# Optimization experiments

Hardware: AMD Instinct MI355X
Metric: run time of the kernel (lower is better)

The kernel has to match this reference:

```python
import jax, jax.numpy as jnp
import numpy as np

SR = 44100
ATTACK_MS = 10.0
RELEASE_MS = 100.0
RATIO_DN = 66.7
RATIO_UP = 0.1
KNEE = 0.1
UP_RANGE_DB = 36.0
TMIN = -40.0
TMAX = 0.0
A_AT = float(np.exp(-1.0 / (ATTACK_MS * SR / 1000.0)))
A_REL = float(np.exp(-1.0 / (RELEASE_MS * SR / 1000.0)))


def smooth_log_level(rect_db):
    # rect_db: [B, N]. Leaky integrator with input-dependent attack/release coeff.
    def step(curr, v):  # curr, v: [B]
        alpha = jnp.where(v > curr, A_AT, A_REL)
        new = alpha * curr + (1.0 - alpha) * v
        return new, new
    _, lv = jax.lax.scan(step, rect_db[:, 0], rect_db.T)  # lv: [N, B]
    return lv.T


def setup_inputs() -> dict:
    key = jax.random.key(0)
    k1, k2 = jax.random.split(key)
    x = jax.random.normal(k1, (16, 441000), dtype=jnp.float32)
    threshold = jax.random.uniform(k2, (16, 1), dtype=jnp.float32)
    depth = jnp.ones((16, 1), dtype=jnp.float32)
    return {"x": x, "threshold": threshold, "depth": depth}


def reference(x, threshold, depth):
    # mode == 'peak'
    rect = jnp.abs(x)
    rect_db = 20.0 * jnp.log10(rect + 1e-8)
    level_db = smooth_log_level(rect_db)  # [B, N]
    thresh_db = TMIN + threshold * (TMAX - TMIN)  # [B, 1]
    diff_dn = level_db - thresh_db
    gain_dn_db = jnp.where(
        diff_dn > -KNEE,
        -(1.0 - 1.0 / RATIO_DN) * 0.5 * (diff_dn + KNEE + jnp.sqrt((diff_dn - KNEE) ** 2 + 1e-4)),
        jnp.zeros_like(diff_dn),
    )
    diff_up = thresh_db - level_db
    raw_gain_up_db = jnp.where(
        diff_up > -KNEE,
        (1.0 - RATIO_UP) * 0.5 * (diff_up + KNEE + jnp.sqrt((diff_up - KNEE) ** 2 + 1e-4)),
        jnp.zeros_like(diff_up),
    )
    gain_up_db = jnp.minimum(raw_gain_up_db, UP_RANGE_DB)
    gain_db = (gain_dn_db + gain_up_db) * depth
    gain = 10.0 ** (gain_db / 20.0)
    return x * gain
```

## Files before the change

kernel.cpp:

```cpp
#include <hip/hip_runtime.h>
#include <math.h>

#define N_SAMP 441000
#define BATCH  16
#define N_OCT  55125
#define OPAD   55296
#define NMG    13824
#define MGF    576
#define MGB    2304
#define NWAVE  54

#define A_AT  0.9977349953069123f
#define A_REL 0.9997732683378945f
#define OMA_AT  (1.0f - A_AT)
#define OMA_REL (1.0f - A_REL)

typedef float vf4 __attribute__((ext_vector_type(4)));

static __device__ __forceinline__ float rect_db_f(float xv) {
    return 6.020599913279624f * log2f(fabsf(xv) + 1e-8f);
}
static __device__ __forceinline__ float step_v(float s, float v) {
    return fmaxf(fmaf(A_AT, s, OMA_AT * v), fmaf(A_REL, s, OMA_REL * v));
}
static __device__ __forceinline__ float max3f(float a, float b, float c) {
    float d;
    asm("v_max3_f32 %0, %1, %2, %3" : "=v"(d) : "v"(a), "v"(b), "v"(c));
    return d;
}
static __device__ __forceinline__ float gain_mul(float s, float th, float dp) {
    float ddn = s - th;
    float gdn = 0.0f;
    if (ddn > -0.1f) {
        float dm = ddn - 0.1f;
        gdn = -0.4925037481259370f * (ddn + 0.1f + sqrtf(fmaf(dm, dm, 1e-4f)));
    }
    float dup = th - s;
    float gup = 0.0f;
    if (dup > -0.1f) {
        float um = dup - 0.1f;
        gup = 0.45f * (dup + 0.1f + sqrtf(fmaf(um, um, 1e-4f)));
    }
    gup = fminf(gup, 36.0f);
    return exp2f((gdn + gup) * dp * 0.1660964047443681f);
}

__global__ __launch_bounds__(256) void coef8_kernel(const float* __restrict__ x,
                                                    float* __restrict__ K) {
    int l = blockIdx.x * 256 + threadIdx.x;
    int slot = l & 3, b = (l >> 2) & 15, mg = l >> 6;
    int o = mg * 4 + slot;
    if (o >= N_OCT) return;
    const float4* xp = (const float4*)(x + (size_t)b * N_SAMP + (size_t)o * 8);
    float4 xa = xp[0], xb = xp[1];
    float vv[8];
    vv[0] = rect_db_f(xa.x); vv[1] = rect_db_f(xa.y);
    vv[2] = rect_db_f(xa.z); vv[3] = rect_db_f(xa.w);
    vv[4] = rect_db_f(xb.x); vv[5] = rect_db_f(xb.y);
    vv[6] = rect_db_f(xb.z); vv[7] = rect_db_f(xb.w);
    float c[9];
    c[0] = OMA_REL * vv[0];
    c[1] = OMA_AT * vv[0];
    #pragma unroll
    for (int j = 1; j < 8; ++j) {
        float p = OMA_AT * vv[j], q = OMA_REL * vv[j];
        c[j + 1] = fmaf(A_AT, c[j], p);
        #pragma unroll
        for (int m = j; m >= 1; --m)
            c[m] = fmaxf(fmaf(A_AT, c[m - 1], p), fmaf(A_REL, c[m], q));
        c[0] = fmaf(A_REL, c[0], q);
    }
    float* kp = K + (size_t)mg * MGF + (b * 4 + slot);
    #pragma unroll
    for (int pl = 0; pl < 9; ++pl) kp[pl * 64] = c[pl];
}

__global__ __launch_bounds__(64, 1) void scan8_kernel(const float* __restrict__ Kf,
                                                      const float* __restrict__ x,
                                                      float* __restrict__ lvl) {
    int wb = blockIdx.x;
    int xcd = wb & 7, jj = wb >> 3;
    int w = (xcd < 6 ? xcd * 7 : 42 + (xcd - 6) * 6) + jj;
    const int lane = threadIdx.x;
    const int grp = lane >> 4, b = lane & 15;
    const int k = 4 * w + grp;

    constexpr double dAT = 0.9977349953069123, dRL = 0.9997732683378945;
    constexpr double dAT2 = dAT * dAT, dAT4 = dAT2 * dAT2;
    constexpr double dRL2 = dRL * dRL, dRL4 = dRL2 * dRL2;
    const float S0 = (float)(dRL4 * dRL4);
    const float S1 = (float)(dAT * dRL4 * dRL2 * dRL);
    const float S2 = (float)(dAT2 * dRL4 * dRL2);
    const float S3 = (float)(dAT2 * dAT * dRL4 * dRL);
    const float S4 = (float)(dAT4 * dRL4);
    const float S5 = (float)(dAT4 * dAT * dRL2 * dRL);
    const float S6 = (float)(dAT4 * dAT2 * dRL2);
    const float S7 = (float)(dAT4 * dAT2 * dAT * dRL);
    const float S8 = (float)(dAT4 * dAT4);

    vf4 R0[9], R1[9], R2[9], R3[9];
    vf4 lv;
    float s;
    unsigned voff;
    float* lq;
    float* dq = lvl + (size_t)16 * OPAD + lane * 4;

#define LDB(R) do {                                                                              \
    asm volatile("global_load_dwordx4 %0, %1, %2 offset:0"    : "=v"(R[0]) : "v"(voff), "s"(Kf)); \
    asm volatile("global_load_dwordx4 %0, %1, %2 offset:256"  : "=v"(R[1]) : "v"(voff), "s"(Kf)); \
    asm volatile("global_load_dwordx4 %0, %1, %2 offset:512"  : "=v"(R[2]) : "v"(voff), "s"(Kf)); \
    asm volatile("global_load_dwordx4 %0, %1, %2 offset:768"  : "=v"(R[3]) : "v"(voff), "s"(Kf)); \
    asm volatile("global_load_dwordx4 %0, %1, %2 offset:1024" : "=v"(R[4]) : "v"(voff), "s"(Kf)); \
    asm volatile("global_load_dwordx4 %0, %1, %2 offset:1280" : "=v"(R[5]) : "v"(voff), "s"(Kf)); \
    asm volatile("global_load_dwordx4 %0, %1, %2 offset:1536" : "=v"(R[6]) : "v"(voff), "s"(Kf)); \
    asm volatile("global_load_dwordx4 %0, %1, %2 offset:1792" : "=v"(R[7]) : "v"(voff), "s"(Kf)); \
    asm volatile("global_load_dwordx4 %0, %1, %2 offset:2048" : "=v"(R[8]) : "v"(voff), "s"(Kf)); \
    voff += MGB;                                                                                  \
} while (0)

#define WAITP() do {                                       \
    asm volatile("s_waitcnt vmcnt(27)" ::: "memory");      \
    __builtin_amdgcn_sched_barrier(0);                     \
} while (0)

#define CMP(R) do {                                        \
    _Pragma("unroll")                                      \
    for (int _e = 0; _e < 4; ++_e) {                       \
        float c0 = fmaf(S0, s, R[0][_e]);                  \
        float c1 = fmaf(S1, s, R[1][_e]);                  \
        float c2 = fmaf(S2, s, R[2][_e]);                  \
        float c3 = fmaf(S3, s, R[3][_e]);                  \
        float c4 = fmaf(S4, s, R[4][_e]);                  \
        float c5 = fmaf(S5, s, R[5][_e]);                  \
        float c6 = fmaf(S6, s, R[6][_e]);                  \
        float c7 = fmaf(S7, s, R[7][_e]);                  \
        float c8 = fmaf(S8, s, R[8][_e]);                  \
        s = max3f(max3f(c0, c1, c2), max3f(c3, c4, c5), max3f(c6, c7, c8)); \
        lv[_e] = s;                                        \
    }                                                      \
} while (0)

#define PH_W(R) do { WAITP(); CMP(R); LDB(R); } while (0)
#define PH_E(R) do { WAITP(); CMP(R);                      \
    lq[0] = lv[0]; lq[16] = lv[1]; lq[32] = lv[2]; lq[48] = lv[3]; lq += 64; \
    LDB(R); } while (0)
#define PH_D(R) do { WAITP(); CMP(R); {                    \
    float* _sp = ((unsigned)(sb - kw) < 64u) ? lq : dq;    \
    _sp[0] = lv[0]; _sp[16] = lv[1]; _sp[32] = lv[2]; _sp[48] = lv[3]; }   \
    lq += 64; ++sb; LDB(R); } while (0)

    if (w >= 4) {
        const int g0 = (k - 16) * 64;
        s = rect_db_f(x[(size_t)b * N_SAMP + (size_t)g0 * 32]);
        asm volatile("" :: "v"(s));
        voff = (unsigned)g0 * MGB + (unsigned)b * 16u;
        LDB(R0); LDB(R1); LDB(R2); LDB(R3);
        #pragma clang loop unroll(disable)
        for (int it = 0; it < 256; ++it) { PH_W(R0); PH_W(R1); PH_W(R2); PH_W(R3); }
        lq = lvl + (size_t)k * 256 * 16 + b;
        #pragma clang loop unroll(disable)
        for (int it = 0; it < 16; ++it) { PH_E(R0); PH_E(R1); PH_E(R2); PH_E(R3); }
    } else {
        const int nit = (4 * w + 4) * 16;
        s = rect_db_f(x[(size_t)b * N_SAMP]);
        asm volatile("" :: "v"(s));
        voff = (unsigned)b * 16u;
        int sb = 0;
        const unsigned kw = (unsigned)(k << 6);
        lq = lvl + b;
        LDB(R0); LDB(R1); LDB(R2); LDB(R3);
        #pragma clang loop unroll(disable)
        for (int it = 0; it < nit; ++it) { PH_D(R0); PH_D(R1); PH_D(R2); PH_D(R3); }
    }
    asm volatile("s_waitcnt vmcnt(0)" ::: "memory");

#undef LDB
#undef WAITP
#undef CMP
#undef PH_W
#undef PH_E
#undef PH_D
}

__global__ __launch_bounds__(256) void out8_kernel(const float* __restrict__ x,
                                                   const float* __restrict__ lvl,
                                                   const float* __restrict__ thr,
                                                   const float* __restrict__ dep,
                                                   float* __restrict__ out) {
    int o = blockIdx.x * 256 + threadIdx.x;
    int b = blockIdx.y;
    if (o >= N_OCT) return;
    const float4* xp = (const float4*)(x + (size_t)b * N_SAMP + (size_t)o * 8);
    float4 xa = xp[0], xb = xp[1];
    float v0 = rect_db_f(xa.x), v1 = rect_db_f(xa.y);
    float v2 = rect_db_f(xa.z), v3 = rect_db_f(xa.w);
    float v4 = rect_db_f(xb.x), v5 = rect_db_f(xb.y);
    float v6 = rect_db_f(xb.z), v7 = rect_db_f(xb.w);
    float s = (o == 0) ? v0 : lvl[(size_t)(o - 1) * 16 + b];
    float l0 = step_v(s, v0);
    float l1 = step_v(l0, v1);
    float l2 = step_v(l1, v2);
    float l3 = step_v(l2, v3);
    float l4 = step_v(l3, v4);
    float l5 = step_v(l4, v5);
    float l6 = step_v(l5, v6);
    float l7 = step_v(l6, v7);
    float th = fmaf(thr[b], 40.0f, -40.0f);
    float dp = dep[b];
    float4 oa, ob;
    oa.x = xa.x * gain_mul(l0, th, dp);
    oa.y = xa.y * gain_mul(l1, th, dp);
    oa.z = xa.z * gain_mul(l2, th, dp);
    oa.w = xa.w * gain_mul(l3, th, dp);
    ob.x = xb.x * gain_mul(l4, th, dp);
    ob.y = xb.y * gain_mul(l5, th, dp);
    ob.z = xb.z * gain_mul(l6, th, dp);
    ob.w = xb.w * gain_mul(l7, th, dp);
    float4* op = (float4*)(out + (size_t)b * N_SAMP + (size_t)o * 8);
    op[0] = oa;
    op[1] = ob;
}

__global__ __launch_bounds__(64) void scan_fused(const float* __restrict__ x,
                                                 const float* __restrict__ thr,
                                                 const float* __restrict__ dep,
                                                 float* __restrict__ out) {
    int t = blockIdx.x * 64 + threadIdx.x;
    const int NCH = 54, CH = 8192, WM = 32768;
    if (t >= BATCH * NCH) return;
    int b = t / NCH, k = t - b * NCH;
    int start = k * CH, end = min(start + CH, N_SAMP), w0 = max(start - WM, 0);
    const float* xr = x + (size_t)b * N_SAMP;
    float th = fmaf(thr[b], 40.0f, -40.0f);
    float dp = dep[b];
    float s = rect_db_f(xr[w0]);
    for (int j = w0; j < start; ++j) s = step_v(s, rect_db_f(xr[j]));
    float* orow = out + (size_t)b * N_SAMP;
    for (int j = start; j < end; ++j) {
        float xv = xr[j];
        s = step_v(s, rect_db_f(xv));
        orow[j] = xv * gain_mul(s, th, dp);
    }
}

extern "C" void kernel_launch(void* const* d_in, const int* in_sizes, int n_in,
                              void* d_out, int out_size, void* d_ws, size_t ws_size,
                              hipStream_t stream) {
    const float* x   = (const float*)d_in[0];
    const float* thr = (const float*)d_in[1];
    const float* dep = (const float*)d_in[2];
    float* out = (float*)d_out;

    const size_t k_bytes   = (size_t)NMG * MGF * sizeof(float);
    const size_t lvl_bytes = ((size_t)16 * OPAD + 512) * sizeof(float);

    if (ws_size >= k_bytes + lvl_bytes) {
        float* K   = (float*)d_ws;
        float* lvl = (float*)((char*)d_ws + k_bytes);
        coef8_kernel<<<(NMG * 64) / 256, 256, 0, stream>>>(x, K);
        scan8_kernel<<<NWAVE, 64, 0, stream>>>(K, x, lvl);
        dim3 gpar((N_OCT + 255) / 256, BATCH);
        out8_kernel<<<gpar, 256, 0, stream>>>(x, lvl, thr, dep, out);
    } else {
        scan_fused<<<(BATCH * 54 + 63) / 64, 64, 0, stream>>>(x, thr, dep, out);
    }
}
```

Before: 253.3 us.

## Stage scan coefficients through LDS with a 7-deep async global-to-LDS pipeline

Replaces the register-resident 4-stage global_load_dwordx4 ring in the sequential scan with global_load_lds staging into a 7-slot shared-memory ring. Each phase then reads the next block from LDS into a double-buffered register set. The goal is a deeper prefetch without the VGPR cost, so the latency-bound serial max-plus scan stalls less on memory. The level buffer layout also changes from [octet][batch] to [batch][octet], so the stores become contiguous vf4 writes, and out8_kernel indexing is updated to match. This adds LDS traffic, extra waitcnt bookkeeping and complex loop-count arithmetic that could mis-cover the tail.

Result: slower. 329.5 us (+30.1%).

```diff
diff --git a/kernel.cpp b/kernel.cpp
--- a/kernel.cpp
+++ b/kernel.cpp
@@ -78,6 +78,8 @@
 __global__ __launch_bounds__(64, 1) void scan8_kernel(const float* __restrict__ Kf,
                                                       const float* __restrict__ x,
                                                       float* __restrict__ lvl) {
+    __shared__ vf4 smem[7 * 576];
+
     int wb = blockIdx.x;
     int xcd = wb & 7, jj = wb >> 3;
     int w = (xcd < 6 ? xcd * 7 : 42 + (xcd - 6) * 6) + jj;
@@ -98,29 +100,25 @@
     const float S7 = (float)(dAT4 * dAT2 * dAT * dRL);
     const float S8 = (float)(dAT4 * dAT4);
 
-    vf4 R0[9], R1[9], R2[9], R3[9];
+    vf4 rA[9], rB[9];
     vf4 lv;
     float s;
-    unsigned voff;
-    float* lq;
+    const char* gp;
+    float* lq = lvl;
     float* dq = lvl + (size_t)16 * OPAD + lane * 4;
-
-#define LDB(R) do {                                                                              \
-    asm volatile("global_load_dwordx4 %0, %1, %2 offset:0"    : "=v"(R[0]) : "v"(voff), "s"(Kf)); \
-    asm volatile("global_load_dwordx4 %0, %1, %2 offset:256"  : "=v"(R[1]) : "v"(voff), "s"(Kf)); \
-    asm volatile("global_load_dwordx4 %0, %1, %2 offset:512"  : "=v"(R[2]) : "v"(voff), "s"(Kf)); \
-    asm volatile("global_load_dwordx4 %0, %1, %2 offset:768"  : "=v"(R[3]) : "v"(voff), "s"(Kf)); \
-    asm volatile("global_load_dwordx4 %0, %1, %2 offset:1024" : "=v"(R[4]) : "v"(voff), "s"(Kf)); \
-    asm volatile("global_load_dwordx4 %0, %1, %2 offset:1280" : "=v"(R[5]) : "v"(voff), "s"(Kf)); \
-    asm volatile("global_load_dwordx4 %0, %1, %2 offset:1536" : "=v"(R[6]) : "v"(voff), "s"(Kf)); \
-    asm volatile("global_load_dwordx4 %0, %1, %2 offset:1792" : "=v"(R[7]) : "v"(voff), "s"(Kf)); \
-    asm volatile("global_load_dwordx4 %0, %1, %2 offset:2048" : "=v"(R[8]) : "v"(voff), "s"(Kf)); \
-    voff += MGB;                                                                                  \
-} while (0)
-
-#define WAITP() do {                                       \
-    asm volatile("s_waitcnt vmcnt(27)" ::: "memory");      \
-    __builtin_amdgcn_sched_barrier(0);                     \
+    int sb = 0;
+    unsigned kw = 0;
+
+#define GLLDS(GPTR, LIDX)                                                        \
+    __builtin_amdgcn_global_load_lds(                                            \
+        (const __attribute__((address_space(1))) void*)(GPTR),                   \
+        (__attribute__((address_space(3))) void*)&smem[(LIDX)], 16, 0, 0)
+
+#define STAGE(SLOT) do {                                                         \
+    _Pragma("unroll")                                                            \
+    for (int _j = 0; _j < 9; ++_j)                                               \
+        GLLDS(gp + _j * 256, (SLOT) * 576 + _j * 64);                            \
+    gp += MGB;                                                                   \
 } while (0)
 
 #define CMP(R) do {                                        \
@@ -140,46 +138,86 @@
     }                                                      \
 } while (0)
 
-#define PH_W(R) do { WAITP(); CMP(R); LDB(R); } while (0)
-#define PH_E(R) do { WAITP(); CMP(R);                      \
-    lq[0] = lv[0]; lq[16] = lv[1]; lq[32] = lv[2]; lq[48] = lv[3]; lq += 64; \
-    LDB(R); } while (0)
-#define PH_D(R) do { WAITP(); CMP(R); {                    \
+#define PH(SLOT, CUR, NXT, ST) do {                                              \
+    asm volatile("s_waitcnt vmcnt(45)" ::: "memory");                            \
+    __builtin_amdgcn_sched_barrier(0);                                           \
+    _Pragma("unroll")                                                            \
+    for (int _j = 0; _j < 9; ++_j)                                               \
+        NXT[_j] = smem[(((SLOT) + 1) % 7) * 576 + _j * 64 + lane];               \
+    CMP(CUR);                                                                    \
+    ST;                                                                          \
+    asm volatile("s_waitcnt lgkmcnt(9)" ::: "memory");                           \
+    STAGE(SLOT);                                                                 \
+} while (0)
+
+#define ST_W ((void)0)
+#define ST_E do { *(vf4*)lq = lv; lq += 4; } while (0)
+#define ST_D do {                                          \
     float* _sp = ((unsigned)(sb - kw) < 64u) ? lq : dq;    \
-    _sp[0] = lv[0]; _sp[16] = lv[1]; _sp[32] = lv[2]; _sp[48] = lv[3]; }   \
-    lq += 64; ++sb; LDB(R); } while (0)
+    *(vf4*)_sp = lv; lq += 4; ++sb;                        \
+} while (0)
+
+#define G14(ST) do { \
+    PH(0,rA,rB,ST); PH(1,rB,rA,ST); PH(2,rA,rB,ST); PH(3,rB,rA,ST); PH(4,rA,rB,ST); PH(5,rB,rA,ST); PH(6,rA,rB,ST); \
+    PH(0,rB,rA,ST); PH(1,rA,rB,ST); PH(2,rB,rA,ST); PH(3,rA,rB,ST); PH(4,rB,rA,ST); PH(5,rA,rB,ST); PH(6,rB,rA,ST); \
+} while (0)
+#define PRE2(ST) do { PH(0,rA,rB,ST); PH(1,rB,rA,ST); } while (0)
+#define G14S2(ST) do { \
+    PH(2,rA,rB,ST); PH(3,rB,rA,ST); PH(4,rA,rB,ST); PH(5,rB,rA,ST); PH(6,rA,rB,ST); PH(0,rB,rA,ST); PH(1,rA,rB,ST); \
+    PH(2,rB,rA,ST); PH(3,rA,rB,ST); PH(4,rB,rA,ST); PH(5,rA,rB,ST); PH(6,rB,rA,ST); PH(0,rA,rB,ST); PH(1,rB,rA,ST); \
+} while (0)
+#define PRE8S2(ST) do { \
+    PH(2,rA,rB,ST); PH(3,rB,rA,ST); PH(4,rA,rB,ST); PH(5,rB,rA,ST); PH(6,rA,rB,ST); PH(0,rB,rA,ST); PH(1,rA,rB,ST); PH(2,rB,rA,ST); \
+} while (0)
+
+#define PROLOG() do {                                                            \
+    _Pragma("unroll")                                                            \
+    for (int _s = 0; _s < 7; ++_s) STAGE(_s);                                    \
+    asm volatile("s_waitcnt vmcnt(54)" ::: "memory");                            \
+    __builtin_amdgcn_sched_barrier(0);                                           \
+    _Pragma("unroll")                                                            \
+    for (int _j = 0; _j < 9; ++_j) rA[_j] = smem[_j * 64 + lane];                \
+} while (0)
 
     if (w >= 4) {
         const int g0 = (k - 16) * 64;
         s = rect_db_f(x[(size_t)b * N_SAMP + (size_t)g0 * 32]);
         asm volatile("" :: "v"(s));
-        voff = (unsigned)g0 * MGB + (unsigned)b * 16u;
-        LDB(R0); LDB(R1); LDB(R2); LDB(R3);
+        gp = (const char*)Kf + (size_t)g0 * MGB + (size_t)b * 16;
+        PROLOG();
         #pragma clang loop unroll(disable)
-        for (int it = 0; it < 256; ++it) { PH_W(R0); PH_W(R1); PH_W(R2); PH_W(R3); }
-        lq = lvl + (size_t)k * 256 * 16 + b;
+        for (int it = 0; it < 73; ++it) G14(ST_W);
+        PRE2(ST_W);
+        lq = lvl + (size_t)b * OPAD + (size_t)k * 256;
         #pragma clang loop unroll(disable)
-        for (int it = 0; it < 16; ++it) { PH_E(R0); PH_E(R1); PH_E(R2); PH_E(R3); }
+        for (int it = 0; it < 4; ++it) G14S2(ST_E);
+        PRE8S2(ST_E);
     } else {
-        const int nit = (4 * w + 4) * 16;
         s = rect_db_f(x[(size_t)b * N_SAMP]);
         asm volatile("" :: "v"(s));
-        voff = (unsigned)b * 16u;
-        int sb = 0;
-        const unsigned kw = (unsigned)(k << 6);
-        lq = lvl + b;
-        LDB(R0); LDB(R1); LDB(R2); LDB(R3);
+        gp = (const char*)Kf + (size_t)b * 16;
+        sb = 0;
+        kw = (unsigned)(k << 6);
+        lq = lvl + (size_t)b * OPAD;
+        PROLOG();
+        const int qs = (256 * (w + 1) + 13) / 14;
         #pragma clang loop unroll(disable)
-        for (int it = 0; it < nit; ++it) { PH_D(R0); PH_D(R1); PH_D(R2); PH_D(R3); }
+        for (int it = 0; it < qs; ++it) G14(ST_D);
     }
     asm volatile("s_waitcnt vmcnt(0)" ::: "memory");
 
-#undef LDB
-#undef WAITP
+#undef GLLDS
+#undef STAGE
 #undef CMP
-#undef PH_W
-#undef PH_E
-#undef PH_D
+#undef PH
+#undef ST_W
+#undef ST_E
+#undef ST_D
+#undef G14
+#undef PRE2
+#undef G14S2
+#undef PRE8S2
+#undef PROLOG
 }
 
 __global__ __launch_bounds__(256) void out8_kernel(const float* __restrict__ x,
@@ -196,7 +234,7 @@
     float v2 = rect_db_f(xa.z), v3 = rect_db_f(xa.w);
     float v4 = rect_db_f(xb.x), v5 = rect_db_f(xb.y);
     float v6 = rect_db_f(xb.z), v7 = rect_db_f(xb.w);
-    float s = (o == 0) ? v0 : lvl[(size_t)(o - 1) * 16 + b];
+    float s = (o == 0) ? v0 : lvl[(size_t)b * OPAD + o - 1];
     float l0 = step_v(s, v0);
     float l1 = step_v(l0, v1);
     float l2 = step_v(l1, v2);
```

## Widen max-plus scan block from 8 to 16 samples per group

Applied to the files above, without the earlier changes.

The precomputed max-plus composition of the attack/release recurrence now covers blocks of 16 samples instead of 8, giving 17 coefficients per block. This halves the number of sequential scan steps and the number of boundary levels stored. The scan kernel uses 27 waves with two buffered loads instead of 54 waves with four, and the level array is laid out per batch row so stores are contiguous vec4 writes. In exchange the coefficient kernel does roughly quadratic more max/fma work per group, each scan step carries a longer max chain, and the scan now runs on fewer waves.

After: 285.8 us. +12.8%, slower.

```diff
diff --git a/kernel.cpp b/kernel.cpp
--- a/kernel.cpp
+++ b/kernel.cpp
@@ -3,12 +3,12 @@
 
 #define N_SAMP 441000
 #define BATCH  16
-#define N_OCT  55125
-#define OPAD   55296
-#define NMG    13824
-#define MGF    576
-#define MGB    2304
-#define NWAVE  54
+#define G_LAST 27562
+#define LPAD   27648
+#define NMG16  6912
+#define MGF16  1088
+#define MGB16  4352
+#define NWAVE  27
 
 #define A_AT  0.9977349953069123f
 #define A_REL 0.9997732683378945f
@@ -45,24 +45,59 @@
     return exp2f((gdn + gup) * dp * 0.1660964047443681f);
 }
 
-__global__ __launch_bounds__(256) void coef8_kernel(const float* __restrict__ x,
-                                                    float* __restrict__ K) {
+constexpr double dpw(double xx, int n) {
+    double r = 1.0;
+    for (int i = 0; i < n; ++i) r *= xx;
+    return r;
+}
+#define DAT 0.9977349953069123
+#define DRL 0.9997732683378945
+constexpr float SC0  = (float)(dpw(DRL, 16));
+constexpr float SC1  = (float)(dpw(DAT, 1)  * dpw(DRL, 15));
+constexpr float SC2  = (float)(dpw(DAT, 2)  * dpw(DRL, 14));
+constexpr float SC3  = (float)(dpw(DAT, 3)  * dpw(DRL, 13));
+constexpr float SC4  = (float)(dpw(DAT, 4)  * dpw(DRL, 12));
+constexpr float SC5  = (float)(dpw(DAT, 5)  * dpw(DRL, 11));
+constexpr float SC6  = (float)(dpw(DAT, 6)  * dpw(DRL, 10));
+constexpr float SC7  = (float)(dpw(DAT, 7)  * dpw(DRL, 9));
+constexpr float SC8  = (float)(dpw(DAT, 8)  * dpw(DRL, 8));
+constexpr float SC9  = (float)(dpw(DAT, 9)  * dpw(DRL, 7));
+constexpr float SC10 = (float)(dpw(DAT, 10) * dpw(DRL, 6));
+constexpr float SC11 = (float)(dpw(DAT, 11) * dpw(DRL, 5));
+constexpr float SC12 = (float)(dpw(DAT, 12) * dpw(DRL, 4));
+constexpr float SC13 = (float)(dpw(DAT, 13) * dpw(DRL, 3));
+constexpr float SC14 = (float)(dpw(DAT, 14) * dpw(DRL, 2));
+constexpr float SC15 = (float)(dpw(DAT, 15) * dpw(DRL, 1));
+constexpr float SC16 = (float)(dpw(DAT, 16));
+
+__global__ __launch_bounds__(256) void coef16_kernel(const float* __restrict__ x,
+                                                     float* __restrict__ K) {
     int l = blockIdx.x * 256 + threadIdx.x;
     int slot = l & 3, b = (l >> 2) & 15, mg = l >> 6;
-    int o = mg * 4 + slot;
-    if (o >= N_OCT) return;
-    const float4* xp = (const float4*)(x + (size_t)b * N_SAMP + (size_t)o * 8);
+    int g = mg * 4 + slot;
+    if (g > G_LAST) return;
+    const float4* xp = (const float4*)(x + (size_t)b * N_SAMP + (size_t)g * 16);
+    float vv[16];
     float4 xa = xp[0], xb = xp[1];
-    float vv[8];
     vv[0] = rect_db_f(xa.x); vv[1] = rect_db_f(xa.y);
     vv[2] = rect_db_f(xa.z); vv[3] = rect_db_f(xa.w);
     vv[4] = rect_db_f(xb.x); vv[5] = rect_db_f(xb.y);
     vv[6] = rect_db_f(xb.z); vv[7] = rect_db_f(xb.w);
-    float c[9];
+    if (g < G_LAST) {
+        float4 xc = xp[2], xd = xp[3];
+        vv[8]  = rect_db_f(xc.x); vv[9]  = rect_db_f(xc.y);
+        vv[10] = rect_db_f(xc.z); vv[11] = rect_db_f(xc.w);
+        vv[12] = rect_db_f(xd.x); vv[13] = rect_db_f(xd.y);
+        vv[14] = rect_db_f(xd.z); vv[15] = rect_db_f(xd.w);
+    } else {
+        #pragma unroll
+        for (int i = 8; i < 16; ++i) vv[i] = vv[7];
+    }
+    float c[17];
     c[0] = OMA_REL * vv[0];
     c[1] = OMA_AT * vv[0];
     #pragma unroll
-    for (int j = 1; j < 8; ++j) {
+    for (int j = 1; j < 16; ++j) {
         float p = OMA_AT * vv[j], q = OMA_REL * vv[j];
         c[j + 1] = fmaf(A_AT, c[j], p);
         #pragma unroll
@@ -70,133 +105,155 @@
             c[m] = fmaxf(fmaf(A_AT, c[m - 1], p), fmaf(A_REL, c[m], q));
         c[0] = fmaf(A_REL, c[0], q);
     }
-    float* kp = K + (size_t)mg * MGF + (b * 4 + slot);
+    float* kp = K + (size_t)mg * MGF16 + (b * 4 + slot);
     #pragma unroll
-    for (int pl = 0; pl < 9; ++pl) kp[pl * 64] = c[pl];
-}
-
-__global__ __launch_bounds__(64, 1) void scan8_kernel(const float* __restrict__ Kf,
-                                                      const float* __restrict__ x,
-                                                      float* __restrict__ lvl) {
+    for (int pl = 0; pl < 17; ++pl) kp[pl * 64] = c[pl];
+}
+
+__global__ __launch_bounds__(64, 1) void scan16_kernel(const float* __restrict__ Kf,
+                                                       const float* __restrict__ x,
+                                                       float* __restrict__ lvl) {
     int wb = blockIdx.x;
     int xcd = wb & 7, jj = wb >> 3;
-    int w = (xcd < 6 ? xcd * 7 : 42 + (xcd - 6) * 6) + jj;
+    int w = (xcd < 3 ? xcd * 4 : 12 + (xcd - 3) * 3) + jj;
     const int lane = threadIdx.x;
     const int grp = lane >> 4, b = lane & 15;
     const int k = 4 * w + grp;
 
-    constexpr double dAT = 0.9977349953069123, dRL = 0.9997732683378945;
-    constexpr double dAT2 = dAT * dAT, dAT4 = dAT2 * dAT2;
-    constexpr double dRL2 = dRL * dRL, dRL4 = dRL2 * dRL2;
-    const float S0 = (float)(dRL4 * dRL4);
-    const float S1 = (float)(dAT * dRL4 * dRL2 * dRL);
-    const float S2 = (float)(dAT2 * dRL4 * dRL2);
-    const float S3 = (float)(dAT2 * dAT * dRL4 * dRL);
-    const float S4 = (float)(dAT4 * dRL4);
-    const float S5 = (float)(dAT4 * dAT * dRL2 * dRL);
-    const float S6 = (float)(dAT4 * dAT2 * dRL2);
-    const float S7 = (float)(dAT4 * dAT2 * dAT * dRL);
-    const float S8 = (float)(dAT4 * dAT4);
-
-    vf4 R0[9], R1[9], R2[9], R3[9];
+    vf4 R0[17], R1[17];
     vf4 lv;
     float s;
-    unsigned voff;
+    unsigned va, vb;
     float* lq;
-    float* dq = lvl + (size_t)16 * OPAD + lane * 4;
+    float* dq = lvl + (size_t)16 * LPAD + lane * 4;
+
+#define SB() __builtin_amdgcn_sched_barrier(0)
 
 #define LDB(R) do {                                                                              \
-    asm volatile("global_load_dwordx4 %0, %1, %2 offset:0"    : "=v"(R[0]) : "v"(voff), "s"(Kf)); \
-    asm volatile("global_load_dwordx4 %0, %1, %2 offset:256"  : "=v"(R[1]) : "v"(voff), "s"(Kf)); \
-    asm volatile("global_load_dwordx4 %0, %1, %2 offset:512"  : "=v"(R[2]) : "v"(voff), "s"(Kf)); \
-    asm volatile("global_load_dwordx4 %0, %1, %2 offset:768"  : "=v"(R[3]) : "v"(voff), "s"(Kf)); \
-    asm volatile("global_load_dwordx4 %0, %1, %2 offset:1024" : "=v"(R[4]) : "v"(voff), "s"(Kf)); \
-    asm volatile("global_load_dwordx4 %0, %1, %2 offset:1280" : "=v"(R[5]) : "v"(voff), "s"(Kf)); \
-    asm volatile("global_load_dwordx4 %0, %1, %2 offset:1536" : "=v"(R[6]) : "v"(voff), "s"(Kf)); \
-    asm volatile("global_load_dwordx4 %0, %1, %2 offset:1792" : "=v"(R[7]) : "v"(voff), "s"(Kf)); \
-    asm volatile("global_load_dwordx4 %0, %1, %2 offset:2048" : "=v"(R[8]) : "v"(voff), "s"(Kf)); \
-    voff += MGB;                                                                                  \
+    asm volatile("global_load_dwordx4 %0, %1, %2 offset:0"    : "=v"(R[0])  : "v"(va), "s"(Kf)); \
+    asm volatile("global_load_dwordx4 %0, %1, %2 offset:256"  : "=v"(R[1])  : "v"(va), "s"(Kf)); \
+    asm volatile("global_load_dwordx4 %0, %1, %2 offset:512"  : "=v"(R[2])  : "v"(va), "s"(Kf)); \
+    asm volatile("global_load_dwordx4 %0, %1, %2 offset:768"  : "=v"(R[3])  : "v"(va), "s"(Kf)); \
+    asm volatile("global_load_dwordx4 %0, %1, %2 offset:1024" : "=v"(R[4])  : "v"(va), "s"(Kf)); \
+    asm volatile("global_load_dwordx4 %0, %1, %2 offset:1280" : "=v"(R[5])  : "v"(va), "s"(Kf)); \
+    asm volatile("global_load_dwordx4 %0, %1, %2 offset:1536" : "=v"(R[6])  : "v"(va), "s"(Kf)); \
+    asm volatile("global_load_dwordx4 %0, %1, %2 offset:1792" : "=v"(R[7])  : "v"(va), "s"(Kf)); \
+    asm volatile("global_load_dwordx4 %0, %1, %2 offset:2048" : "=v"(R[8])  : "v"(va), "s"(Kf)); \
+    asm volatile("global_load_dwordx4 %0, %1, %2 offset:0"    : "=v"(R[9])  : "v"(vb), "s"(Kf)); \
+    asm volatile("global_load_dwordx4 %0, %1, %2 offset:256"  : "=v"(R[10]) : "v"(vb), "s"(Kf)); \
+    asm volatile("global_load_dwordx4 %0, %1, %2 offset:512"  : "=v"(R[11]) : "v"(vb), "s"(Kf)); \
+    asm volatile("global_load_dwordx4 %0, %1, %2 offset:768"  : "=v"(R[12]) : "v"(vb), "s"(Kf)); \
+    asm volatile("global_load_dwordx4 %0, %1, %2 offset:1024" : "=v"(R[13]) : "v"(vb), "s"(Kf)); \
+    asm volatile("global_load_dwordx4 %0, %1, %2 offset:1280" : "=v"(R[14]) : "v"(vb), "s"(Kf)); \
+    asm volatile("global_load_dwordx4 %0, %1, %2 offset:1536" : "=v"(R[15]) : "v"(vb), "s"(Kf)); \
+    asm volatile("global_load_dwordx4 %0, %1, %2 offset:1792" : "=v"(R[16]) : "v"(vb), "s"(Kf)); \
+    va += MGB16;                                                                                 \
+    vb += MGB16;                                                                                 \
 } while (0)
 
-#define WAITP() do {                                       \
-    asm volatile("s_waitcnt vmcnt(27)" ::: "memory");      \
-    __builtin_amdgcn_sched_barrier(0);                     \
+#define WAIT17() do {                                      \
+    asm volatile("s_waitcnt vmcnt(17)" ::: "memory");      \
+    SB();                                                  \
 } while (0)
 
 #define CMP(R) do {                                        \
     _Pragma("unroll")                                      \
     for (int _e = 0; _e < 4; ++_e) {                       \
-        float c0 = fmaf(S0, s, R[0][_e]);                  \
-        float c1 = fmaf(S1, s, R[1][_e]);                  \
-        float c2 = fmaf(S2, s, R[2][_e]);                  \
-        float c3 = fmaf(S3, s, R[3][_e]);                  \
-        float c4 = fmaf(S4, s, R[4][_e]);                  \
-        float c5 = fmaf(S5, s, R[5][_e]);                  \
-        float c6 = fmaf(S6, s, R[6][_e]);                  \
-        float c7 = fmaf(S7, s, R[7][_e]);                  \
-        float c8 = fmaf(S8, s, R[8][_e]);                  \
-        s = max3f(max3f(c0, c1, c2), max3f(c3, c4, c5), max3f(c6, c7, c8)); \
+        float c0  = fmaf(SC0,  s, R[0][_e]);               \
+        float c1  = fmaf(SC1,  s, R[1][_e]);               \
+        float c2  = fmaf(SC2,  s, R[2][_e]);               \
+        float c3  = fmaf(SC3,  s, R[3][_e]);               \
+        float c4  = fmaf(SC4,  s, R[4][_e]);               \
+        float c5  = fmaf(SC5,  s, R[5][_e]);               \
+        float c6  = fmaf(SC6,  s, R[6][_e]);               \
+        float c7  = fmaf(SC7,  s, R[7][_e]);               \
+        float c8  = fmaf(SC8,  s, R[8][_e]);               \
+        float c9  = fmaf(SC9,  s, R[9][_e]);               \
+        float c10 = fmaf(SC10, s, R[10][_e]);              \
+        float c11 = fmaf(SC11, s, R[11][_e]);              \
+        float c12 = fmaf(SC12, s, R[12][_e]);              \
+        float c13 = fmaf(SC13, s, R[13][_e]);              \
+        float c14 = fmaf(SC14, s, R[14][_e]);              \
+        float c15 = fmaf(SC15, s, R[15][_e]);              \
+        float c16 = fmaf(SC16, s, R[16][_e]);              \
+        float t0 = max3f(c0, c1, c2);                      \
+        float t1 = max3f(c3, c4, c5);                      \
+        float t2 = max3f(c6, c7, c8);                      \
+        float t3 = max3f(c9, c10, c11);                    \
+        float t4 = max3f(c12, c13, c14);                   \
+        s = max3f(max3f(t0, t1, t2), max3f(t3, t4, c15), c16); \
         lv[_e] = s;                                        \
     }                                                      \
 } while (0)
 
-#define PH_W(R) do { WAITP(); CMP(R); LDB(R); } while (0)
-#define PH_E(R) do { WAITP(); CMP(R);                      \
-    lq[0] = lv[0]; lq[16] = lv[1]; lq[32] = lv[2]; lq[48] = lv[3]; lq += 64; \
-    LDB(R); } while (0)
-#define PH_D(R) do { WAITP(); CMP(R); {                    \
+#define ST_W ((void)0)
+#define ST_E do { *(vf4*)lq = lv; lq += 4; } while (0)
+#define ST_D do {                                          \
     float* _sp = ((unsigned)(sb - kw) < 64u) ? lq : dq;    \
-    _sp[0] = lv[0]; _sp[16] = lv[1]; _sp[32] = lv[2]; _sp[48] = lv[3]; }   \
-    lq += 64; ++sb; LDB(R); } while (0)
-
-    if (w >= 4) {
-        const int g0 = (k - 16) * 64;
-        s = rect_db_f(x[(size_t)b * N_SAMP + (size_t)g0 * 32]);
+    *(vf4*)_sp = lv; lq += 4; ++sb;                        \
+} while (0)
+
+#define PH_A(ST) do { WAIT17(); CMP(R0); ST; SB(); LDB(R0); SB(); } while (0)
+#define PH_B(ST) do { WAIT17(); CMP(R1); ST; SB(); LDB(R1); SB(); } while (0)
+
+#define PROLOG() do { LDB(R0); LDB(R1); SB(); } while (0)
+
+    if (w >= 2) {
+        const int mg0 = (k - 8) * 64;
+        s = rect_db_f(x[(size_t)b * N_SAMP + (size_t)mg0 * 64]);
         asm volatile("" :: "v"(s));
-        voff = (unsigned)g0 * MGB + (unsigned)b * 16u;
-        LDB(R0); LDB(R1); LDB(R2); LDB(R3);
+        va = (unsigned)mg0 * MGB16 + (unsigned)b * 16u;
+        vb = va + 2304u;
+        PROLOG();
         #pragma clang loop unroll(disable)
-        for (int it = 0; it < 256; ++it) { PH_W(R0); PH_W(R1); PH_W(R2); PH_W(R3); }
-        lq = lvl + (size_t)k * 256 * 16 + b;
+        for (int it = 0; it < 256; ++it) { PH_A(ST_W); PH_B(ST_W); }
+        lq = lvl + (size_t)b * LPAD + (size_t)k * 256;
         #pragma clang loop unroll(disable)
-        for (int it = 0; it < 16; ++it) { PH_E(R0); PH_E(R1); PH_E(R2); PH_E(R3); }
+        for (int it = 0; it < 32; ++it) { PH_A(ST_E); PH_B(ST_E); }
     } else {
-        const int nit = (4 * w + 4) * 16;
         s = rect_db_f(x[(size_t)b * N_SAMP]);
         asm volatile("" :: "v"(s));
-        voff = (unsigned)b * 16u;
+        va = (unsigned)b * 16u;
+        vb = va + 2304u;
         int sb = 0;
-        const unsigned kw = (unsigned)(k << 6);
-        lq = lvl + b;
-        LDB(R0); LDB(R1); LDB(R2); LDB(R3);
+        const unsigned kw = (unsigned)(k * 64);
+        lq = lvl + (size_t)b * LPAD;
+        PROLOG();
+        const int np = (4 * w + 4) * 32;
         #pragma clang loop unroll(disable)
-        for (int it = 0; it < nit; ++it) { PH_D(R0); PH_D(R1); PH_D(R2); PH_D(R3); }
+        for (int it = 0; it < np; ++it) { PH_A(ST_D); PH_B(ST_D); }
     }
     asm volatile("s_waitcnt vmcnt(0)" ::: "memory");
 
+#undef SB
 #undef LDB
-#undef WAITP
+#undef WAIT17
 #undef CMP
-#undef PH_W
-#undef PH_E
-#undef PH_D
-}
-
-__global__ __launch_bounds__(256) void out8_kernel(const float* __restrict__ x,
-                                                   const float* __restrict__ lvl,
-                                                   const float* __restrict__ thr,
-                                                   const float* __restrict__ dep,
-                                                   float* __restrict__ out) {
-    int o = blockIdx.x * 256 + threadIdx.x;
+#undef ST_W
+#undef ST_E
+#undef ST_D
+#undef PH_A
+#undef PH_B
+#undef PROLOG
+}
+
+__global__ __launch_bounds__(256) void out16_kernel(const float* __restrict__ x,
+                                                    const float* __restrict__ lvl,
+                                                    const float* __restrict__ thr,
+                                                    const float* __restrict__ dep,
+                                                    float* __restrict__ out) {
+    int g = blockIdx.x * 256 + threadIdx.x;
     int b = blockIdx.y;
-    if (o >= N_OCT) return;
-    const float4* xp = (const float4*)(x + (size_t)b * N_SAMP + (size_t)o * 8);
+    if (g > G_LAST) return;
+    const float4* xp = (const float4*)(x + (size_t)b * N_SAMP + (size_t)g * 16);
     float4 xa = xp[0], xb = xp[1];
     float v0 = rect_db_f(xa.x), v1 = rect_db_f(xa.y);
     float v2 = rect_db_f(xa.z), v3 = rect_db_f(xa.w);
     float v4 = rect_db_f(xb.x), v5 = rect_db_f(xb.y);
     float v6 = rect_db_f(xb.z), v7 = rect_db_f(xb.w);
-    float s = (o == 0) ? v0 : lvl[(size_t)(o - 1) * 16 + b];
+    float s = (g == 0) ? v0 : lvl[(size_t)b * LPAD + g - 1];
+    float th = fmaf(thr[b], 40.0f, -40.0f);
+    float dp = dep[b];
     float l0 = step_v(s, v0);
     float l1 = step_v(l0, v1);
     float l2 = step_v(l1, v2);
@@ -205,8 +262,6 @@
     float l5 = step_v(l4, v5);
     float l6 = step_v(l5, v6);
     float l7 = step_v(l6, v7);
-    float th = fmaf(thr[b], 40.0f, -40.0f);
-    float dp = dep[b];
     float4 oa, ob;
     oa.x = xa.x * gain_mul(l0, th, dp);
     oa.y = xa.y * gain_mul(l1, th, dp);
@@ -216,9 +271,35 @@
     ob.y = xb.y * gain_mul(l5, th, dp);
     ob.z = xb.z * gain_mul(l6, th, dp);
     ob.w = xb.w * gain_mul(l7, th, dp);
-    float4* op = (float4*)(out + (size_t)b * N_SAMP + (size_t)o * 8);
+    float4* op = (float4*)(out + (size_t)b * N_SAMP + (size_t)g * 16);
     op[0] = oa;
     op[1] = ob;
+    if (g < G_LAST) {
+        float4 xc = xp[2], xd = xp[3];
+        float v8  = rect_db_f(xc.x), v9  = rect_db_f(xc.y);
+        float v10 = rect_db_f(xc.z), v11 = rect_db_f(xc.w);
+        float v12 = rect_db_f(xd.x), v13 = rect_db_f(xd.y);
+        float v14 = rect_db_f(xd.z), v15 = rect_db_f(xd.w);
+        float l8  = step_v(l7, v8);
+        float l9  = step_v(l8, v9);
+        float l10 = step_v(l9, v10);
+        float l11 = step_v(l10, v11);
+        float l12 = step_v(l11, v12);
+        float l13 = step_v(l12, v13);
+        float l14 = step_v(l13, v14);
+        float l15 = step_v(l14, v15);
+        float4 oc, od;
+        oc.x = xc.x * gain_mul(l8,  th, dp);
+        oc.y = xc.y * gain_mul(l9,  th, dp);
+        oc.z = xc.z * gain_mul(l10, th, dp);
+        oc.w = xc.w * gain_mul(l11, th, dp);
+        od.x = xd.x * gain_mul(l12, th, dp);
+        od.y = xd.y * gain_mul(l13, th, dp);
+        od.z = xd.z * gain_mul(l14, th, dp);
+        od.w = xd.w * gain_mul(l15, th, dp);
+        op[2] = oc;
+        op[3] = od;
+    }
 }
 
 __global__ __launch_bounds__(64) void scan_fused(const float* __restrict__ x,
@@ -251,16 +332,16 @@
     const float* dep = (const float*)d_in[2];
     float* out = (float*)d_out;
 
-    const size_t k_bytes   = (size_t)NMG * MGF * sizeof(float);
-    const size_t lvl_bytes = ((size_t)16 * OPAD + 512) * sizeof(float);
+    const size_t k_bytes   = (size_t)NMG16 * MGF16 * sizeof(float);
+    const size_t lvl_bytes = ((size_t)16 * LPAD + 512) * sizeof(float);
 
     if (ws_size >= k_bytes + lvl_bytes) {
         float* K   = (float*)d_ws;
         float* lvl = (float*)((char*)d_ws + k_bytes);
-        coef8_kernel<<<(NMG * 64) / 256, 256, 0, stream>>>(x, K);
-        scan8_kernel<<<NWAVE, 64, 0, stream>>>(K, x, lvl);
-        dim3 gpar((N_OCT + 255) / 256, BATCH);
-        out8_kernel<<<gpar, 256, 0, stream>>>(x, lvl, thr, dep, out);
+        coef16_kernel<<<(NMG16 * 64) / 256, 256, 0, stream>>>(x, K);
+        scan16_kernel<<<NWAVE, 64, 0, stream>>>(K, x, lvl);
+        dim3 gpar((G_LAST + 1 + 255) / 256, BATCH);
+        out16_kernel<<<gpar, 256, 0, stream>>>(x, lvl, thr, dep, out);
     } else {
         scan_fused<<<(BATCH * 54 + 63) / 64, 64, 0, stream>>>(x, thr, dep, out);
     }
```
